# Performance work log

Hardware: AMD Instinct MI355X
Metric: run time of the kernel (lower is better)

Reference implementation:

```python
import jax, jax.numpy as jnp
import numpy as np

N, E, C, H = 100000, 3200000, 4, 64
EPS = 1e-8


def setup_inputs() -> dict:
    key = jax.random.key(0)
    k1, k2, k3, k4, k5, k6, k7 = jax.random.split(key, 7)
    x = jax.random.uniform(k1, (N, C), dtype=jnp.float32)            # [pm10, u10, v10, aux]
    pos = jax.random.normal(k2, (N, 2), dtype=jnp.float32)           # node coordinates
    edge_index = jax.random.randint(k3, (2, E), 0, N, dtype=jnp.int64)
    # PhysicsFluxLayer edge MLP: in = [x_i, x_j, wind_proj, dist] -> hidden
    fan_in = 2 * C + 2
    mlp_w = jax.random.normal(k4, (H, fan_in), dtype=jnp.float32) / np.sqrt(fan_in)
    mlp_b = jnp.zeros((H,), dtype=jnp.float32)
    # output head (module inits to zero; use small random values for a non-degenerate baseline)
    head_w = jax.random.normal(k5, (1, H), dtype=jnp.float32) * 0.02
    head_b = jax.random.normal(k6, (1,), dtype=jnp.float32) * 0.02
    return {"x": x, "pos": pos, "mlp_w": mlp_w, "mlp_b": mlp_b,
            "head_w": head_w, "head_b": head_b, "edge_index": edge_index}


def reference(x, pos, mlp_w, mlp_b, head_w, head_b, edge_index):
    src = edge_index[0]   # j (message source)
    dst = edge_index[1]   # i (message target)
    u10, v10 = x[:, 1], x[:, 2]
    # edge geometry: direction i -> j and distance
    d = pos[src] - pos[dst]                                  # [E,2]
    dist = jnp.sqrt(jnp.sum(d * d, axis=1) + EPS)            # [E]
    dhat = d / dist[:, None]
    # source wind projected onto the edge direction (advective transport term)
    wind_proj = u10[src] * dhat[:, 0] + v10[src] * dhat[:, 1]  # [E]
    edge_feat = jnp.concatenate(
        [x[dst], x[src], wind_proj[:, None], dist[:, None]], axis=1)  # [E, 2C+2]
    msg = jax.nn.relu(edge_feat @ mlp_w.T + mlp_b)            # [E,H]
    flux = jax.ops.segment_sum(msg, dst, num_segments=N)      # [N,H] scatter-add
    delta_pm10 = flux @ head_w.T + head_b                     # [N,1]
    pm10_next = jax.nn.softplus(x[:, 0:1] + delta_pm10)       # [N,1]
    return pm10_next, delta_pm10
```

## Files before the change

kernel.cpp:

```cpp
#include <hip/hip_runtime.h>
#include <hip/hip_bf16.h>


#define HID    64
#define EPSV   1e-8f
#define BNODES 256
#define CAP    10240
#define MAXB   512
#define BLK_SC 512
#define RPT_SC 25
#define LSTAGE (BLK_SC * RPT_SC)
#define BLK_C  256
#define SLOTW  20
#define OVF_CAP 65536

typedef _Float16 half8 __attribute__((ext_vector_type(8)));
typedef _Float16 half2_t __attribute__((ext_vector_type(2)));
typedef float f32x4 __attribute__((ext_vector_type(4)));

__device__ __forceinline__ unsigned int packh2(float a, float b) {
    union { half2_t h; unsigned int u; } v;
    v.h = half2_t{(_Float16)a, (_Float16)b};
    return v.u;
}

__device__ __forceinline__ void feat_from_rows(float4 xs, float4 ps4,
                                               float4 xd, float4 pd4,
                                               float* f) {
    float d0 = ps4.x - pd4.x;
    float d1 = ps4.y - pd4.y;
    float dist = sqrtf(fmaf(d0, d0, fmaf(d1, d1, EPSV)));
    float inv = 1.0f / dist;
    float wind = (xs.y * d0 + xs.z * d1) * inv;
    f[0] = xd.x; f[1] = xd.y; f[2] = xd.z; f[3] = xd.w;
    f[4] = xs.x; f[5] = xs.y; f[6] = xs.z; f[7] = xs.w;
    f[8] = wind; f[9] = dist;
}

__device__ __forceinline__ float mlp_scalar_g(const float* __restrict__ mlp_w,
                                              const float* __restrict__ mlp_b,
                                              const float* __restrict__ head_w,
                                              const float* f) {
    float sacc = 0.0f;
    for (int h = 0; h < HID; h++) {
        const float* wr = mlp_w + h * 10;
        float a = mlp_b[h];
        a = fmaf(wr[0], f[0], a); a = fmaf(wr[1], f[1], a);
        a = fmaf(wr[2], f[2], a); a = fmaf(wr[3], f[3], a);
        a = fmaf(wr[4], f[4], a); a = fmaf(wr[5], f[5], a);
        a = fmaf(wr[6], f[6], a); a = fmaf(wr[7], f[7], a);
        a = fmaf(wr[8], f[8], a); a = fmaf(wr[9], f[9], a);
        a = fmaxf(a, 0.0f);
        sacc = fmaf(head_w[h], a, sacc);
    }
    return sacc;
}

__global__ __launch_bounds__(BLK_SC) void scatter_kernel(
    const int* __restrict__ srcs, const int* __restrict__ dsts,
    int E, int B, int N,
    const float4* __restrict__ x, const float2* __restrict__ pos,
    const float* __restrict__ mlp_w,
    float4* __restrict__ xpos, uint4* __restrict__ wbuf,
    unsigned long long* g_ptr64, unsigned int* __restrict__ sorted,
    int2* __restrict__ ovf, int* ovf_cnt)
{
    __shared__ int hist[MAXB];
    __shared__ int base[MAXB];
    __shared__ int pfx[MAXB];
    __shared__ int wsum[BLK_SC / 64];
    __shared__ unsigned int lpay[LSTAGE];
    __shared__ unsigned int ldst[LSTAGE];

    int tid  = threadIdx.x;
    int lane = tid & 63;
    int wid  = tid >> 6;
    int lo = blockIdx.x * LSTAGE;

    int es[RPT_SC], ed[RPT_SC];
    bool ev[RPT_SC];
    #pragma unroll
    for (int r = 0; r < RPT_SC; r++) {
        int e = lo + r * BLK_SC + tid;
        bool okr = (e < E);
        ev[r] = okr;
        int ee = okr ? e : 0;
        es[r] = srcs[ee];
        ed[r] = dsts[ee];
    }

    for (int b2 = tid; b2 < MAXB; b2 += BLK_SC) hist[b2] = 0;

    {
        int nper = (N + gridDim.x - 1) / gridDim.x;
        int n0 = blockIdx.x * nper;
        int n1 = min(n0 + nper, N);
        for (int n = n0 + tid; n < n1; n += BLK_SC) {
            float4 xr = x[n];
            float2 pr = pos[n];
            xpos[2 * n]     = xr;
            xpos[2 * n + 1] = make_float4(pr.x, pr.y, 0.0f, 0.0f);
        }
    }
    if (blockIdx.x == 0 && tid < 64) {
        int colw = tid & 15, quadw = tid >> 4;
        #pragma unroll
        for (int c = 0; c < 4; c++) {
            int h = c * 16 + colw;
            half8 wf = half8{0, 0, 0, 0, 0, 0, 0, 0};
            if (quadw == 0) {
                #pragma unroll
                for (int j = 0; j < 8; j++) wf[j] = (_Float16)mlp_w[h * 10 + j];
            } else if (quadw == 1) {
                wf[0] = (_Float16)mlp_w[h * 10 + 8];
                wf[1] = (_Float16)mlp_w[h * 10 + 9];
            }
            union { half8 h8; uint4 u4; } cv;
            cv.h8 = wf;
            wbuf[c * 64 + tid] = cv.u4;
        }
    }
    __syncthreads();

    #pragma unroll
    for (int r = 0; r < RPT_SC; r++) {
        if (ev[r]) {
            int b = ed[r] >> 8;
            int rk = atomicAdd(&hist[b], 1);
            es[r] = (es[r] << 8) | (ed[r] & 255);
            ed[r] = (b << 14) | rk;
        }
    }
    __syncthreads();

    int PB = (B + 1) >> 1;
    for (int p = tid; p < PB; p += BLK_SC) {
        int b0 = 2 * p, b1 = 2 * p + 1;
        unsigned long long h0 = (unsigned int)hist[b0];
        unsigned long long h1 = (b1 < B) ? (unsigned int)hist[b1] : 0ull;
        unsigned long long comb = h0 | (h1 << 32);
        unsigned long long old = 0ull;
        if (comb) old = atomicAdd(&g_ptr64[p], comb);
        base[b0] = (int)(old & 0xffffffffull);
        if (b1 < B) base[b1] = (int)(old >> 32);
    }
    int v = hist[tid];
    int xs_ = v;
    #pragma unroll
    for (int m = 1; m < 64; m <<= 1) {
        int y = __shfl_up(xs_, m, 64);
        if (lane >= m) xs_ += y;
    }
    if (lane == 63) wsum[wid] = xs_;
    __syncthreads();
    if (tid == 0) {
        int a = 0;
        #pragma unroll
        for (int j = 0; j < BLK_SC / 64; j++) { int t = wsum[j]; wsum[j] = a; a += t; }
    }
    __syncthreads();
    pfx[tid] = wsum[wid] + xs_ - v;
    __syncthreads();

    #pragma unroll
    for (int r = 0; r < RPT_SC; r++) {
        if (ev[r]) {
            int b  = ed[r] >> 14;
            int rk = ed[r] & 0x3FFF;
            int p  = pfx[b] + rk;
            unsigned int pay = (unsigned int)es[r];
            lpay[p] = pay;
            int rel = base[b] + rk;
            if (rel < CAP) {
                ldst[p] = (unsigned int)b * CAP + (unsigned int)rel;
            } else {
                ldst[p] = 0xFFFFFFFFu;
                int o = atomicAdd(ovf_cnt, 1);
                if (o < OVF_CAP)
                    ovf[o] = make_int2((int)(pay >> 8), (b << 8) | (int)(pay & 255u));
            }
        }
    }
    __syncthreads();

    int cnt_blk = min(E - lo, LSTAGE);
    for (int t = tid; t < cnt_blk; t += BLK_SC) {
        unsigned int d = ldst[t];
        if (d != 0xFFFFFFFFu) sorted[d] = lpay[t];
    }
}

__global__ __launch_bounds__(BLK_C, 4) void compute_kernel(
    const float4* __restrict__ xpos,
    const uint4* __restrict__ wbuf,
    const float* __restrict__ mlp_w, const float* __restrict__ mlp_b,
    const float* __restrict__ head_w,
    const unsigned int* __restrict__ sorted,
    const unsigned long long* __restrict__ g_ptr64,
    const int2* __restrict__ ovf, const int* __restrict__ ovf_cnt,
    float* __restrict__ partial, int BB, int ksh, int N)
{
    __shared__ __align__(16) unsigned int stage[4 * 64 * SLOTW];
    __shared__ __align__(16) float4 drows[2 * BNODES];
    __shared__ float acc[BNODES];
    int tid  = threadIdx.x;
    int wave = tid >> 6;
    int lane = tid & 63;
    int col  = lane & 15;
    int quad = lane >> 4;
    int wbase = wave * 64 * SLOTW;

    int b    = blockIdx.x >> ksh;
    int part = blockIdx.x & ((1 << ksh) - 1);
    int nbase = b << 8;

    acc[tid] = 0.0f;

    {
        int lim = 2 * N - 1;
        drows[tid]       = xpos[min(2 * nbase + tid, lim)];
        drows[tid + 256] = xpos[min(2 * nbase + tid + 256, lim)];
    }

    {
        unsigned int* slotp = &stage[wbase + lane * SLOTW];
        slotp[5] = 0u;
        *(uint2*)(slotp + 6) = make_uint2(0u, 0u);
        *(uint4*)(slotp + 8) = make_uint4(0u, 0u, 0u, 0u);
        *(uint4*)(slotp + 12) = make_uint4(0u, 0u, 0u, 0u);
    }

    half8 wfr[4];
    f32x4 bias4[4], hw4[4];
    #pragma unroll
    for (int c = 0; c < 4; c++) {
        union { uint4 u4; half8 h8; } cv;
        cv.u4 = wbuf[c * 64 + lane];
        wfr[c] = cv.h8;
        bias4[c] = *(const f32x4*)&mlp_b[c * 16 + quad * 4];
        hw4[c]   = *(const f32x4*)&head_w[c * 16 + quad * 4];
    }
    __syncthreads();

    unsigned long long gp = g_ptr64[b >> 1];
    int cnt = (b & 1) ? (int)(gp >> 32) : (int)(gp & 0xffffffffull);
    cnt = min(cnt, CAP);
    int e0 = (cnt * part) >> ksh;
    int e1 = (cnt * (part + 1)) >> ksh;
    const unsigned int* sp = sorted + (size_t)b * CAP;

    if (e0 < e1) {
        unsigned int p0, p1, p2;
        float4 xA, pA, xB, pB, xC, pC;
        {
            int i = e0 + tid;
            p0 = sp[(i < e1) ? i : e0];
            int i1 = i + BLK_C;
            p1 = sp[(i1 < e1) ? i1 : e0];
            int s0 = (int)(p0 >> 8);
            xA = xpos[2 * s0];
            pA = xpos[2 * s0 + 1];
        }

        auto body = [&](int i0, unsigned int pc, unsigned int pn,
                        unsigned int& pn2, float4 xc, float4 psc,
                        float4& xn, float4& psn) {
            bool cok = (i0 + tid) < e1;
            int dl = (int)(pc & 255u);
            int i2 = i0 + 2 * BLK_C + tid;
            pn2 = sp[(i2 < e1) ? i2 : e0];
            int sn = (int)(pn >> 8);
            xn  = xpos[2 * sn];
            psn = xpos[2 * sn + 1];
            float4 xd  = drows[2 * dl];
            float4 pd4 = drows[2 * dl + 1];
            float f[10];
            feat_from_rows(xc, psc, xd, pd4, f);
            unsigned int* slotp = &stage[wbase + lane * SLOTW];
            *(uint4*)slotp = make_uint4(packh2(f[0], f[1]), packh2(f[2], f[3]),
                                        packh2(f[4], f[5]), packh2(f[6], f[7]));
            slotp[4] = packh2(f[8], f[9]);

            float mysum = 0.0f;
            #pragma unroll
            for (int eg = 0; eg < 4; eg++) {
                const half8 fb = *(const half8*)&stage[wbase + (eg * 16 + col) * SLOTW + quad * 4];
                float sacc = 0.0f;
                #pragma unroll
                for (int c = 0; c < 4; c++) {
                    f32x4 d = __builtin_amdgcn_mfma_f32_16x16x32_f16(wfr[c], fb, bias4[c], 0, 0, 0);
                    sacc = fmaf(hw4[c][0], fmaxf(d[0], 0.f), sacc);
                    sacc = fmaf(hw4[c][1], fmaxf(d[1], 0.f), sacc);
                    sacc = fmaf(hw4[c][2], fmaxf(d[2], 0.f), sacc);
                    sacc = fmaf(hw4[c][3], fmaxf(d[3], 0.f), sacc);
                }
                sacc += __shfl_xor(sacc, 16, 64);
                sacc += __shfl_xor(sacc, 32, 64);
                if (quad == eg) mysum = sacc;
            }
            if (cok) atomicAdd(&acc[dl], mysum);
        };

        int i0 = e0;
        for (;;) {
            body(i0, p0, p1, p2, xA, pA, xB, pB);
            i0 += BLK_C; if (i0 >= e1) break;
            body(i0, p1, p2, p0, xB, pB, xC, pC);
            i0 += BLK_C; if (i0 >= e1) break;
            body(i0, p2, p0, p1, xC, pC, xA, pA);
            i0 += BLK_C; if (i0 >= e1) break;
        }
    }
    __syncthreads();
    partial[(size_t)part * BB + nbase + tid] = acc[tid];

    if (part == 0) {
        __syncthreads();
        int oc = min(*ovf_cnt, OVF_CAP);
        for (int idx = tid; idx < oc; idx += BLK_C) {
            int2 sd = ovf[idx];
            if ((sd.y >> 8) == b) {
                float f[10];
                feat_from_rows(xpos[2 * sd.x], xpos[2 * sd.x + 1],
                               xpos[2 * sd.y], xpos[2 * sd.y + 1], f);
                unsafeAtomicAdd(&partial[sd.y], mlp_scalar_g(mlp_w, mlp_b, head_w, f));
            }
        }
    }
}

__global__ __launch_bounds__(512) void final_kernel(
    const float* __restrict__ xf,
    const float* __restrict__ partial, int BB,
    const float* __restrict__ head_b,
    float* __restrict__ out, int N, int kpart)
{
    int n = blockIdx.x * 512 + threadIdx.x;
    if (n >= N) return;
    float delta = head_b[0];
    for (int p = 0; p < kpart; p++)
        delta += partial[(size_t)p * BB + n];
    float v = xf[4 * n] + delta;
    float sp = fmaxf(v, 0.0f) + log1pf(expf(-fabsf(v)));
    out[n] = sp;
    out[N + n] = delta;
}

__global__ __launch_bounds__(256) void edge_kernel_fallback(
    const float4* __restrict__ x, const float2* __restrict__ pos,
    const float* __restrict__ mlp_w, const float* __restrict__ mlp_b,
    const float* __restrict__ head_w,
    const int* __restrict__ srcs, const int* __restrict__ dsts,
    float* __restrict__ delta_acc, int E)
{
    long e = (long)blockIdx.x * 256 + threadIdx.x;
    if (e >= E) return;
    int s = srcs[e], d = dsts[e];
    float4 xs = x[s], xd = x[d];
    float2 ps = pos[s], pd = pos[d];
    float f[10];
    feat_from_rows(xs, make_float4(ps.x, ps.y, 0, 0),
                   xd, make_float4(pd.x, pd.y, 0, 0), f);
    unsafeAtomicAdd(&delta_acc[d], mlp_scalar_g(mlp_w, mlp_b, head_w, f));
}

__global__ __launch_bounds__(256) void node_kernel_fallback(
    const float* __restrict__ xf, const float* __restrict__ delta_acc,
    const float* __restrict__ head_b, float* __restrict__ out, int N)
{
    int n = blockIdx.x * 256 + threadIdx.x;
    if (n >= N) return;
    float delta = delta_acc[n] + head_b[0];
    float v = xf[4 * n] + delta;
    float sp = fmaxf(v, 0.0f) + log1pf(expf(-fabsf(v)));
    out[n] = sp;
    out[N + n] = delta;
}

static inline size_t align_up(size_t v, size_t a) { return (v + a - 1) & ~(a - 1); }

extern "C" void kernel_launch(void* const* d_in, const int* in_sizes, int n_in,
                              void* d_out, int out_size, void* d_ws, size_t ws_size,
                              hipStream_t stream) {
    const float4* x      = (const float4*)d_in[0];
    const float2* pos    = (const float2*)d_in[1];
    const float*  mlp_w  = (const float*)d_in[2];
    const float*  mlp_b  = (const float*)d_in[3];
    const float*  head_w = (const float*)d_in[4];
    const float*  head_b = (const float*)d_in[5];
    const int*    ei     = (const int*)d_in[6];

    int N = in_sizes[0] / 4;
    int E = in_sizes[6] / 2;
    const int* srcs = ei;
    const int* dsts = ei + E;
    int B  = (N + BNODES - 1) / BNODES;
    int PB = (B + 1) >> 1;
    int BB = B * BNODES;

    size_t off = 0;
    unsigned long long* g_ptr64 = (unsigned long long*)((char*)d_ws + off);
    off = align_up(off + (size_t)PB * 8, 64);
    int* ovf_cnt = (int*)((char*)d_ws + off);
    size_t zero_bytes = off + 64;
    off = align_up(off + 64, 256);
    float4* xpos = (float4*)((char*)d_ws + off);
    off = align_up(off + (size_t)N * 32, 256);
    uint4* wbuf = (uint4*)((char*)d_ws + off);
    off = align_up(off + (size_t)4 * 64 * 16, 256);
    int2* ovf = (int2*)((char*)d_ws + off);
    off = align_up(off + (size_t)OVF_CAP * 8, 256);
    unsigned int* sorted = (unsigned int*)((char*)d_ws + off);
    off = align_up(off + (size_t)B * CAP * 4, 256);
    float* partial = (float*)((char*)d_ws + off);

    int kpart = 8, ksh = 3;
    if (off + (size_t)8 * BB * 4 > ws_size) { kpart = 4; ksh = 2; }
    size_t off_end = off + (size_t)kpart * BB * 4;
    bool fast = (off_end <= ws_size) && (B <= MAXB);

    if (fast) {
        hipMemsetAsync(d_ws, 0, zero_bytes, stream);
        int sgrid = (E + LSTAGE - 1) / LSTAGE;
        scatter_kernel<<<sgrid, BLK_SC, 0, stream>>>(
            srcs, dsts, E, B, N, x, pos, mlp_w,
            xpos, wbuf, g_ptr64, sorted, ovf, ovf_cnt);
        compute_kernel<<<B << ksh, BLK_C, 0, stream>>>(
            xpos, wbuf, mlp_w, mlp_b, head_w, sorted, g_ptr64,
            ovf, ovf_cnt, partial, BB, ksh, N);
        final_kernel<<<(N + 511) / 512, 512, 0, stream>>>(
            (const float*)x, partial, BB, head_b, (float*)d_out, N, kpart);
    } else {
        float* delta = (float*)d_ws;
        hipMemsetAsync(delta, 0, (size_t)N * sizeof(float), stream);
        edge_kernel_fallback<<<(int)((E + 255) / 256), 256, 0, stream>>>(
            x, pos, mlp_w, mlp_b, head_w, srcs, dsts, delta, E);
        node_kernel_fallback<<<(N + 255) / 256, 256, 0, stream>>>(
            (const float*)x, delta, head_b, (float*)d_out, N);
    }
}
```

Before: 144.4 us.

## Fuse final node pass into compute kernel and shrink LDS staging for occupancy

The separate final kernel is removed. Each node bucket now counts its finished compute blocks with a global atomic, and the last block to finish sums the partials and applies the softplus head. The scatter stage per block is halved (RPT_SC 25→12) and the MFMA staging slot width shrinks from 20 to 12 words, with the upper K half of the fragment zero-filled in registers instead of being read from LDS. Launch bounds are raised so more blocks fit per CU. This removes one kernel launch and the re-read of partials. In exchange it adds a completion counter that must be zeroed every call, fence ordering that the last-block reduction depends on, and more scatter blocks doing smaller, less coalesced writes into the sorted buffer.

```diff
diff --git a/kernel.cpp b/kernel.cpp
--- a/kernel.cpp
+++ b/kernel.cpp
@@ -8,10 +8,10 @@
 #define CAP    10240
 #define MAXB   512
 #define BLK_SC 512
-#define RPT_SC 25
+#define RPT_SC 12
 #define LSTAGE (BLK_SC * RPT_SC)
 #define BLK_C  256
-#define SLOTW  20
+#define SLOTW  12
 #define OVF_CAP 65536
 
 typedef _Float16 half8 __attribute__((ext_vector_type(8)));
@@ -56,7 +56,7 @@
     return sacc;
 }
 
-__global__ __launch_bounds__(BLK_SC) void scatter_kernel(
+__global__ __launch_bounds__(BLK_SC, 4) void scatter_kernel(
     const int* __restrict__ srcs, const int* __restrict__ dsts,
     int E, int B, int N,
     const float4* __restrict__ x, const float2* __restrict__ pos,
@@ -190,19 +190,21 @@
     }
 }
 
-__global__ __launch_bounds__(BLK_C, 4) void compute_kernel(
+__global__ __launch_bounds__(BLK_C, 6) void compute_kernel(
     const float4* __restrict__ xpos,
     const uint4* __restrict__ wbuf,
     const float* __restrict__ mlp_w, const float* __restrict__ mlp_b,
-    const float* __restrict__ head_w,
+    const float* __restrict__ head_w, const float* __restrict__ head_b,
     const unsigned int* __restrict__ sorted,
     const unsigned long long* __restrict__ g_ptr64,
     const int2* __restrict__ ovf, const int* __restrict__ ovf_cnt,
-    float* __restrict__ partial, int BB, int ksh, int N)
+    float* __restrict__ partial, int* __restrict__ bdone,
+    float* __restrict__ out, int BB, int ksh, int N)
 {
     __shared__ __align__(16) unsigned int stage[4 * 64 * SLOTW];
     __shared__ __align__(16) float4 drows[2 * BNODES];
     __shared__ float acc[BNODES];
+    __shared__ int lastflag;
     int tid  = threadIdx.x;
     int wave = tid >> 6;
     int lane = tid & 63;
@@ -225,9 +227,8 @@
     {
         unsigned int* slotp = &stage[wbase + lane * SLOTW];
         slotp[5] = 0u;
-        *(uint2*)(slotp + 6) = make_uint2(0u, 0u);
-        *(uint4*)(slotp + 8) = make_uint4(0u, 0u, 0u, 0u);
-        *(uint4*)(slotp + 12) = make_uint4(0u, 0u, 0u, 0u);
+        slotp[6] = 0u;
+        slotp[7] = 0u;
     }
 
     half8 wfr[4];
@@ -284,7 +285,9 @@
             float mysum = 0.0f;
             #pragma unroll
             for (int eg = 0; eg < 4; eg++) {
-                const half8 fb = *(const half8*)&stage[wbase + (eg * 16 + col) * SLOTW + quad * 4];
+                half8 fb = half8{0, 0, 0, 0, 0, 0, 0, 0};
+                if (quad < 2)
+                    fb = *(const half8*)&stage[wbase + (eg * 16 + col) * SLOTW + quad * 4];
                 float sacc = 0.0f;
                 #pragma unroll
                 for (int c = 0; c < 4; c++) {
@@ -315,7 +318,6 @@
     partial[(size_t)part * BB + nbase + tid] = acc[tid];
 
     if (part == 0) {
-        __syncthreads();
         int oc = min(*ovf_cnt, OVF_CAP);
         for (int idx = tid; idx < oc; idx += BLK_C) {
             int2 sd = ovf[idx];
@@ -327,23 +329,28 @@
             }
         }
     }
-}
-
-__global__ __launch_bounds__(512) void final_kernel(
-    const float* __restrict__ xf,
-    const float* __restrict__ partial, int BB,
-    const float* __restrict__ head_b,
-    float* __restrict__ out, int N, int kpart)
-{
-    int n = blockIdx.x * 512 + threadIdx.x;
-    if (n >= N) return;
-    float delta = head_b[0];
-    for (int p = 0; p < kpart; p++)
-        delta += partial[(size_t)p * BB + n];
-    float v = xf[4 * n] + delta;
-    float sp = fmaxf(v, 0.0f) + log1pf(expf(-fabsf(v)));
-    out[n] = sp;
-    out[N + n] = delta;
+
+    __threadfence();
+    __syncthreads();
+    if (tid == 0) {
+        int prev = atomicAdd(&bdone[b], 1);
+        lastflag = (prev == (1 << ksh) - 1) ? 1 : 0;
+    }
+    __syncthreads();
+    if (lastflag) {
+        __threadfence();
+        int n = nbase + tid;
+        if (n < N) {
+            int kp = 1 << ksh;
+            float delta = head_b[0];
+            for (int p = 0; p < kp; p++)
+                delta += partial[(size_t)p * BB + n];
+            float v = drows[2 * tid].x + delta;
+            float sp = fmaxf(v, 0.0f) + log1pf(expf(-fabsf(v)));
+            out[n] = sp;
+            out[N + n] = delta;
+        }
+    }
 }
 
 __global__ __launch_bounds__(256) void edge_kernel_fallback(
@@ -402,8 +409,11 @@
     unsigned long long* g_ptr64 = (unsigned long long*)((char*)d_ws + off);
     off = align_up(off + (size_t)PB * 8, 64);
     int* ovf_cnt = (int*)((char*)d_ws + off);
-    size_t zero_bytes = off + 64;
-    off = align_up(off + 64, 256);
+    off += 64;
+    int* bdone = (int*)((char*)d_ws + off);
+    off += (size_t)MAXB * 4;
+    size_t zero_bytes = off;
+    off = align_up(off, 256);
     float4* xpos = (float4*)((char*)d_ws + off);
     off = align_up(off + (size_t)N * 32, 256);
     uint4* wbuf = (uint4*)((char*)d_ws + off);
@@ -414,9 +424,9 @@
     off = align_up(off + (size_t)B * CAP * 4, 256);
     float* partial = (float*)((char*)d_ws + off);
 
-    int kpart = 8, ksh = 3;
-    if (off + (size_t)8 * BB * 4 > ws_size) { kpart = 4; ksh = 2; }
-    size_t off_end = off + (size_t)kpart * BB * 4;
+    int ksh = 3;
+    if (off + (size_t)8 * BB * 4 > ws_size) ksh = 2;
+    size_t off_end = off + (size_t)(1 << ksh) * BB * 4;
     bool fast = (off_end <= ws_size) && (B <= MAXB);
 
     if (fast) {
@@ -426,10 +436,8 @@
             srcs, dsts, E, B, N, x, pos, mlp_w,
             xpos, wbuf, g_ptr64, sorted, ovf, ovf_cnt);
         compute_kernel<<<B << ksh, BLK_C, 0, stream>>>(
-            xpos, wbuf, mlp_w, mlp_b, head_w, sorted, g_ptr64,
-            ovf, ovf_cnt, partial, BB, ksh, N);
-        final_kernel<<<(N + 511) / 512, 512, 0, stream>>>(
-            (const float*)x, partial, BB, head_b, (float*)d_out, N, kpart);
+            xpos, wbuf, mlp_w, mlp_b, head_w, head_b, sorted, g_ptr64,
+            ovf, ovf_cnt, partial, bdone, (float*)d_out, BB, ksh, N);
     } else {
         float* delta = (float*)d_ws;
         hipMemsetAsync(delta, 0, (size_t)N * sizeof(float), stream);
```

Result: slower. 565.3 us (+291.4%).
